# Kernel tuning notes

Measured on AMD Instinct MI355X. Metric: run time of the kernel, lower is better.

Reference implementation:

```python
import jax, jax.numpy as jnp
import numpy as np

KERNEL_MUL = 2.0
KERNEL_NUM = 5


def setup_inputs() -> dict:
    key = jax.random.key(0)
    k1, k2 = jax.random.split(key)
    source = jax.random.normal(k1, (4096, 256), dtype=jnp.float32)
    target = jax.random.normal(k2, (4096, 256), dtype=jnp.float32)
    return {"source": source, "target": target}


def reference(source, target):
    n = source.shape[0]
    m = target.shape[0]
    total = jnp.concatenate([source, target], axis=0)  # [n+m, d]
    N = n + m
    # pairwise squared L2 distances via GEMM identity (same math as expand-based)
    sq = jnp.sum(total * total, axis=1)  # [N]
    d2 = sq[:, None] + sq[None, :] - 2.0 * (total @ total.T)  # [N, N]
    d2 = jnp.maximum(d2, 0.0)
    # bandwidth from detached distances (torch uses L2_distance.data)
    bandwidth = jax.lax.stop_gradient(jnp.sum(d2)) / (N * N - N)
    bandwidth = bandwidth / (KERNEL_MUL ** (KERNEL_NUM // 2))
    kernels = jnp.zeros_like(d2)
    for i in range(KERNEL_NUM):  # fixed small loop over bandwidths
        kernels = kernels + jnp.exp(-d2 / (bandwidth * (KERNEL_MUL ** i)))
    XX = jnp.mean(kernels[:n, :n])
    YY = jnp.mean(kernels[n:, n:])
    XY = jnp.mean(kernels[:n, n:])
    YX = jnp.mean(kernels[n:, :n])
    return XX + YY - XY - YX
```

## Files before the change

kernel.cpp:

```cpp
#include <hip/hip_runtime.h>
#include <hip/hip_bf16.h>
#include <stdint.h>
#include <math.h>

#define D     256
#define NTOT  8192
#define NSRC  4096
#define NT    64
#define NTRI  (NT * (NT + 1) / 2)
#define PREPB 256

using bf16x8 = __attribute__((ext_vector_type(8))) short;
using f32x4  = __attribute__((ext_vector_type(4))) float;

#define GLB_AS __attribute__((address_space(1)))
#define LDS_AS __attribute__((address_space(3)))

#if __has_builtin(__builtin_amdgcn_exp2f)
#define EXP2F __builtin_amdgcn_exp2f
#else
#define EXP2F exp2f
#endif

#define OFF_XB   ((size_t)0)
#define OFF_SQ   ((size_t)NTOT * D * 2)
#define OFF_CP   (OFF_SQ + (size_t)NTOT * 4)
#define OFF_SP   (OFF_CP + (size_t)PREPB * 256 * 4)
#define OFF_CF   (OFF_SP + (size_t)PREPB * 4)
#define OFF_PT   (OFF_CF + 32)
#define OFF_END  (OFF_PT + (size_t)NTRI * 4)

__global__ __launch_bounds__(256) void prep_kernel(
    const float* __restrict__ src, const float* __restrict__ tgt,
    __hip_bfloat16* __restrict__ xb, float* __restrict__ sq,
    float* __restrict__ colpart, float* __restrict__ sqpart)
{
  __shared__ float scol4[4][256];
  __shared__ float sSl[4];
  const int tid = threadIdx.x, wave = tid >> 6, lane = tid & 63;
  const int row0 = blockIdx.x * 32 + wave * 8;
  const float* p0 = (row0 < NSRC) ? (src + (size_t)row0 * D)
                                  : (tgt + (size_t)(row0 - NSRC) * D);
  float c0 = 0.f, c1 = 0.f, c2 = 0.f, c3 = 0.f, swave = 0.f;
  for (int rr = 0; rr < 8; ++rr) {
    const int row = row0 + rr;
    const float4 v = reinterpret_cast<const float4*>(p0 + (size_t)rr * D)[lane];
    const __hip_bfloat16 b0 = __float2bfloat16(v.x), b1 = __float2bfloat16(v.y),
                         b2 = __float2bfloat16(v.z), b3 = __float2bfloat16(v.w);
    ushort4 h;
    h.x = *(const unsigned short*)&b0; h.y = *(const unsigned short*)&b1;
    h.z = *(const unsigned short*)&b2; h.w = *(const unsigned short*)&b3;
    reinterpret_cast<ushort4*>(xb + (size_t)row * D)[lane] = h;
    const float f0 = __bfloat162float(b0), f1 = __bfloat162float(b1),
                f2 = __bfloat162float(b2), f3 = __bfloat162float(b3);
    c0 += f0; c1 += f1; c2 += f2; c3 += f3;
    float s = f0 * f0 + f1 * f1 + f2 * f2 + f3 * f3;
    #pragma unroll
    for (int off = 32; off > 0; off >>= 1) s += __shfl_down(s, off);
    if (lane == 0) { sq[row] = s; swave += s; }
  }
  scol4[wave][lane * 4 + 0] = c0;
  scol4[wave][lane * 4 + 1] = c1;
  scol4[wave][lane * 4 + 2] = c2;
  scol4[wave][lane * 4 + 3] = c3;
  if (lane == 0) sSl[wave] = swave;
  __syncthreads();
  colpart[blockIdx.x * 256 + tid] =
      scol4[0][tid] + scol4[1][tid] + scol4[2][tid] + scol4[3][tid];
  if (tid == 0) sqpart[blockIdx.x] = sSl[0] + sSl[1] + sSl[2] + sSl[3];
}

__global__ __launch_bounds__(256) void bw_kernel(
    const float* __restrict__ colpart, const float* __restrict__ sqpart,
    float* __restrict__ cf)
{
  __shared__ float red[256];
  const int t = threadIdx.x;
  float cs = 0.f;
  for (int b = 0; b < PREPB; ++b) cs += colpart[b * 256 + t];
  red[t] = cs * cs;
  __syncthreads();
  for (int off = 128; off > 0; off >>= 1) {
    if (t < off) red[t] += red[t + off];
    __syncthreads();
  }
  const float s2 = red[0];
  __syncthreads();
  red[t] = (t < PREPB) ? sqpart[t] : 0.f;
  __syncthreads();
  for (int off = 128; off > 0; off >>= 1) {
    if (t < off) red[t] += red[t + off];
    __syncthreads();
  }
  if (t == 0) {
    const double sumd2 = 2.0 * (double)NTOT * (double)red[0] - 2.0 * (double)s2;
    const double bw = sumd2 / ((double)NTOT * (double)NTOT - (double)NTOT) / 4.0;
    cf[0] = (float)(-1.4426950408889634 / (bw * 16.0));
  }
}

__global__ __launch_bounds__(256) void pair_kernel(
    const __hip_bfloat16* __restrict__ xb, const float* __restrict__ sq,
    const float* __restrict__ cf, float* __restrict__ part)
{
  const int idx = (blockIdx.x & 7) * (NTRI / 8) + (blockIdx.x >> 3);
  const float rr = sqrtf(4160.25f - 2.0f * (float)idx);
  int bi = (int)(64.5f - rr);
  while (NT * (bi + 1) - (bi + 1) * bi / 2 <= idx) ++bi;
  while (NT * bi - bi * (bi - 1) / 2 > idx) --bi;
  const int bj = bi + (idx - (NT * bi - bi * (bi - 1) / 2));

  __shared__ __align__(16) short lA[128 * 64];
  __shared__ __align__(16) short lB[128 * 64];
  __shared__ float sqA[128], sqB[128], wsum[4];

  const int tid = threadIdx.x, wave = tid >> 6, lane = tid & 63;
  const int wr = wave >> 1, wc = wave & 1;

  const float c4 = cf[0];
  if (tid < 128) sqA[tid] = sq[bi * 128 + tid];
  else           sqB[tid - 128] = sq[bj * 128 + (tid - 128)];

  const int srow = lane >> 3;
  const int scol_e = ((lane & 7) ^ srow) * 8;
  const __hip_bfloat16* gA = xb + (size_t)(bi * 128 + wave * 8 + srow) * D + scol_e;
  const __hip_bfloat16* gB = xb + (size_t)(bj * 128 + wave * 8 + srow) * D + scol_e;
  char* ldsA = (char*)lA + (wave * 8) * 128;
  char* ldsB = (char*)lB + (wave * 8) * 128;

  f32x4 acc[4][4];
  #pragma unroll
  for (int mi = 0; mi < 4; ++mi)
    #pragma unroll
    for (int nj = 0; nj < 4; ++nj)
      acc[mi][nj] = (f32x4){0.f, 0.f, 0.f, 0.f};

  #pragma unroll
  for (int t = 0; t < 4; ++t) {
    #pragma unroll
    for (int q = 0; q < 4; ++q) {
      __builtin_amdgcn_global_load_lds(
          (const GLB_AS uint32_t*)(gA + (size_t)q * 32 * D + t * 64),
          (LDS_AS uint32_t*)(ldsA + q * 32 * 128), 16, 0, 0);
      __builtin_amdgcn_global_load_lds(
          (const GLB_AS uint32_t*)(gB + (size_t)q * 32 * D + t * 64),
          (LDS_AS uint32_t*)(ldsB + q * 32 * 128), 16, 0, 0);
    }
    __syncthreads();

    #pragma unroll
    for (int ks = 0; ks < 2; ++ks) {
      bf16x8 af[4], bfr[4];
      const int kb = (ks * 32 + (lane >> 4) * 8) * 2;
      #pragma unroll
      for (int mi = 0; mi < 4; ++mi) {
        const int row = wr * 64 + mi * 16 + (lane & 15);
        af[mi] = *(const bf16x8*)((const char*)lA + row * 128 + (kb ^ ((row & 7) << 4)));
      }
      #pragma unroll
      for (int nj = 0; nj < 4; ++nj) {
        const int row = wc * 64 + nj * 16 + (lane & 15);
        bfr[nj] = *(const bf16x8*)((const char*)lB + row * 128 + (kb ^ ((row & 7) << 4)));
      }
      #pragma unroll
      for (int mi = 0; mi < 4; ++mi)
        #pragma unroll
        for (int nj = 0; nj < 4; ++nj)
          acc[mi][nj] = __builtin_amdgcn_mfma_f32_16x16x32_bf16(
              af[mi], bfr[nj], acc[mi][nj], 0, 0, 0);
    }
    if (t < 3) __syncthreads();
  }

  const int r0 = (lane >> 4) * 4, cc = lane & 15;
  float sjv[4];
  #pragma unroll
  for (int nj = 0; nj < 4; ++nj) sjv[nj] = sqB[wc * 64 + nj * 16 + cc];
  float tsum = 0.f;
  #pragma unroll
  for (int mi = 0; mi < 4; ++mi) {
    #pragma unroll
    for (int r = 0; r < 4; ++r) {
      const float si = sqA[wr * 64 + mi * 16 + r0 + r];
      #pragma unroll
      for (int nj = 0; nj < 4; ++nj) {
        float d2 = fmaf(-2.f, acc[mi][nj][r], si + sjv[nj]);
        d2 = fmaxf(d2, 0.f);
        const float e4 = EXP2F(d2 * c4);
        const float e3 = e4 * e4, e2 = e3 * e3;
        const float e1 = e2 * e2, e0 = e1 * e1;
        tsum += ((e4 + e3) + (e2 + e1)) + e0;
      }
    }
  }
  #pragma unroll
  for (int off = 32; off > 0; off >>= 1) tsum += __shfl_down(tsum, off);
  if (lane == 0) wsum[wave] = tsum;
  __syncthreads();
  if (tid == 0) part[idx] = wsum[0] + wsum[1] + wsum[2] + wsum[3];
}

__global__ __launch_bounds__(256) void out_kernel(
    const float* __restrict__ part, float* __restrict__ out)
{
  __shared__ double red0[256], red1[256], red2[256];
  const int t = threadIdx.x;
  double a0 = 0.0, a1 = 0.0, a2 = 0.0;
  for (int j = t; j < NTRI; j += 256) {
    const float r1 = sqrtf(4160.25f - 2.0f * (float)j);
    int bi = (int)(64.5f - r1);
    while (NT * (bi + 1) - (bi + 1) * bi / 2 <= j) ++bi;
    while (NT * bi - bi * (bi - 1) / 2 > j) --bi;
    const int bj = bi + (j - (NT * bi - bi * (bi - 1) / 2));
    const double w = (bi == bj) ? 1.0 : 2.0;
    const double v = w * (double)part[j];
    if (bi >= 32) a1 += v;
    else if (bj >= 32) a2 += v;
    else a0 += v;
  }
  red0[t] = a0; red1[t] = a1; red2[t] = a2;
  __syncthreads();
  for (int off = 128; off > 0; off >>= 1) {
    if (t < off) {
      red0[t] += red0[t + off];
      red1[t] += red1[t + off];
      red2[t] += red2[t + off];
    }
    __syncthreads();
  }
  if (t == 0)
    out[0] = (float)((red0[0] + red1[0] - red2[0]) /
                     ((double)NSRC * (double)NSRC));
}

extern "C" void kernel_launch(void* const* d_in, const int* in_sizes, int n_in,
                              void* d_out, int out_size, void* d_ws, size_t ws_size,
                              hipStream_t stream) {
  (void)in_sizes; (void)n_in; (void)out_size; (void)ws_size;
  const float* src = (const float*)d_in[0];
  const float* tgt = (const float*)d_in[1];
  char* ws = (char*)d_ws;
  __hip_bfloat16* xb = (__hip_bfloat16*)(ws + OFF_XB);
  float* sq      = (float*)(ws + OFF_SQ);
  float* colpart = (float*)(ws + OFF_CP);
  float* sqpart  = (float*)(ws + OFF_SP);
  float* cf      = (float*)(ws + OFF_CF);
  float* part    = (float*)(ws + OFF_PT);

  prep_kernel<<<PREPB, 256, 0, stream>>>(src, tgt, xb, sq, colpart, sqpart);
  bw_kernel<<<1, 256, 0, stream>>>(colpart, sqpart, cf);
  pair_kernel<<<NTRI, 256, 0, stream>>>(xb, sq, cf, part);
  out_kernel<<<1, 256, 0, stream>>>(part, (float*)d_out);
}
```

Baseline: 56.33 us.

## Quantize inputs to FP8 e4m3 and use fp8 MFMA for pairwise Gram tiles

Replaces the bf16 conversion with a software FP8 e4m3 quantizer in the prep kernel, and uses 16x16x32 fp8 MFMA in the pair kernel. Halving the element size halves global and LDS traffic and cuts the K-loop to two stages, with the staging layout and LDS swizzle rewritten for 128-byte rows. Squared norms and column sums are computed from the dequantized values to stay consistent. This costs a lot of precision, because e4m3 has a 3-bit mantissa, so the kernel exponentials and the final MMD value may drift past tolerance.

```diff
diff --git a/kernel.cpp b/kernel.cpp
--- a/kernel.cpp
+++ b/kernel.cpp
@@ -10,8 +10,7 @@
 #define NTRI  (NT * (NT + 1) / 2)
 #define PREPB 256
 
-using bf16x8 = __attribute__((ext_vector_type(8))) short;
-using f32x4  = __attribute__((ext_vector_type(4))) float;
+using f32x4 = __attribute__((ext_vector_type(4))) float;
 
 #define GLB_AS __attribute__((address_space(1)))
 #define LDS_AS __attribute__((address_space(3)))
@@ -22,8 +21,27 @@
 #define EXP2F exp2f
 #endif
 
+__device__ inline unsigned char f32_to_e4m3(float v) {
+  uint32_t u = __float_as_uint(v);
+  uint32_t s = (u >> 24) & 0x80u;
+  uint32_t m = u & 0x7FFFFFFFu;
+  if (m <= 0x3C000000u) return (unsigned char)s;
+  if (m <  0x3C800000u) return (unsigned char)(s | 0x08u);
+  if (m >= 0x43F00000u) return (unsigned char)(s | 0x7Eu);
+  uint32_t r = m + 0x0007FFFFu + ((m >> 20) & 1u);
+  uint32_t e = (r >> 23) - 127u + 7u;
+  return (unsigned char)(s | (e << 3) | ((r >> 20) & 7u));
+}
+__device__ inline float e4m3_to_f32(unsigned char q) {
+  uint32_t s = ((uint32_t)(q & 0x80u)) << 24;
+  uint32_t em = q & 0x7Fu;
+  if (em == 0) return __uint_as_float(s);
+  uint32_t e = (em >> 3) + 120u;
+  return __uint_as_float(s | (e << 23) | ((em & 7u) << 20));
+}
+
 #define OFF_XB   ((size_t)0)
-#define OFF_SQ   ((size_t)NTOT * D * 2)
+#define OFF_SQ   ((size_t)NTOT * D)
 #define OFF_CP   (OFF_SQ + (size_t)NTOT * 4)
 #define OFF_SP   (OFF_CP + (size_t)PREPB * 256 * 4)
 #define OFF_CF   (OFF_SP + (size_t)PREPB * 4)
@@ -32,7 +50,7 @@
 
 __global__ __launch_bounds__(256) void prep_kernel(
     const float* __restrict__ src, const float* __restrict__ tgt,
-    __hip_bfloat16* __restrict__ xb, float* __restrict__ sq,
+    unsigned char* __restrict__ xb, float* __restrict__ sq,
     float* __restrict__ colpart, float* __restrict__ sqpart)
 {
   __shared__ float scol4[4][256];
@@ -45,14 +63,12 @@
   for (int rr = 0; rr < 8; ++rr) {
     const int row = row0 + rr;
     const float4 v = reinterpret_cast<const float4*>(p0 + (size_t)rr * D)[lane];
-    const __hip_bfloat16 b0 = __float2bfloat16(v.x), b1 = __float2bfloat16(v.y),
-                         b2 = __float2bfloat16(v.z), b3 = __float2bfloat16(v.w);
-    ushort4 h;
-    h.x = *(const unsigned short*)&b0; h.y = *(const unsigned short*)&b1;
-    h.z = *(const unsigned short*)&b2; h.w = *(const unsigned short*)&b3;
-    reinterpret_cast<ushort4*>(xb + (size_t)row * D)[lane] = h;
-    const float f0 = __bfloat162float(b0), f1 = __bfloat162float(b1),
-                f2 = __bfloat162float(b2), f3 = __bfloat162float(b3);
+    uchar4 h;
+    h.x = f32_to_e4m3(v.x); h.y = f32_to_e4m3(v.y);
+    h.z = f32_to_e4m3(v.z); h.w = f32_to_e4m3(v.w);
+    reinterpret_cast<uchar4*>(xb + (size_t)row * D)[lane] = h;
+    const float f0 = e4m3_to_f32(h.x), f1 = e4m3_to_f32(h.y),
+                f2 = e4m3_to_f32(h.z), f3 = e4m3_to_f32(h.w);
     c0 += f0; c1 += f1; c2 += f2; c3 += f3;
     float s = f0 * f0 + f1 * f1 + f2 * f2 + f3 * f3;
     #pragma unroll
@@ -100,7 +116,7 @@
 }
 
 __global__ __launch_bounds__(256) void pair_kernel(
-    const __hip_bfloat16* __restrict__ xb, const float* __restrict__ sq,
+    const unsigned char* __restrict__ xb, const float* __restrict__ sq,
     const float* __restrict__ cf, float* __restrict__ part)
 {
   const int idx = (blockIdx.x & 7) * (NTRI / 8) + (blockIdx.x >> 3);
@@ -110,8 +126,8 @@
   while (NT * bi - bi * (bi - 1) / 2 > idx) --bi;
   const int bj = bi + (idx - (NT * bi - bi * (bi - 1) / 2));
 
-  __shared__ __align__(16) short lA[128 * 64];
-  __shared__ __align__(16) short lB[128 * 64];
+  __shared__ __align__(16) unsigned char lA[128 * 128];
+  __shared__ __align__(16) unsigned char lB[128 * 128];
   __shared__ float sqA[128], sqB[128], wsum[4];
 
   const int tid = threadIdx.x, wave = tid >> 6, lane = tid & 63;
@@ -121,12 +137,23 @@
   if (tid < 128) sqA[tid] = sq[bi * 128 + tid];
   else           sqB[tid - 128] = sq[bj * 128 + (tid - 128)];
 
-  const int srow = lane >> 3;
-  const int scol_e = ((lane & 7) ^ srow) * 8;
-  const __hip_bfloat16* gA = xb + (size_t)(bi * 128 + wave * 8 + srow) * D + scol_e;
-  const __hip_bfloat16* gB = xb + (size_t)(bj * 128 + wave * 8 + srow) * D + scol_e;
-  char* ldsA = (char*)lA + (wave * 8) * 128;
-  char* ldsB = (char*)lB + (wave * 8) * 128;
+  const unsigned char* gA0 =
+      xb + (size_t)(bi * 128 + wave * 32 + (lane >> 3)) * D + ((lane & 7) ^ (lane >> 3)) * 16;
+  const unsigned char* gB0 =
+      xb + (size_t)(bj * 128 + wave * 32 + (lane >> 3)) * D + ((lane & 7) ^ (lane >> 3)) * 16;
+  char* dA = (char*)lA + wave * 4096;
+  char* dB = (char*)lB + wave * 4096;
+
+#define STAGE(t) do {                                                        \
+    _Pragma("unroll")                                                        \
+    for (int q = 0; q < 4; ++q) {                                            \
+      __builtin_amdgcn_global_load_lds(                                      \
+          (const GLB_AS uint32_t*)(gA0 + (size_t)q * 8 * D + (t) * 128),     \
+          (LDS_AS uint32_t*)(dA + q * 1024), 16, 0, 0);                      \
+      __builtin_amdgcn_global_load_lds(                                      \
+          (const GLB_AS uint32_t*)(gB0 + (size_t)q * 8 * D + (t) * 128),     \
+          (LDS_AS uint32_t*)(dB + q * 1024), 16, 0, 0);                      \
+    } } while (0)
 
   f32x4 acc[4][4];
   #pragma unroll
@@ -135,44 +162,41 @@
     for (int nj = 0; nj < 4; ++nj)
       acc[mi][nj] = (f32x4){0.f, 0.f, 0.f, 0.f};
 
-  #pragma unroll
-  for (int t = 0; t < 4; ++t) {
-    #pragma unroll
-    for (int q = 0; q < 4; ++q) {
-      __builtin_amdgcn_global_load_lds(
-          (const GLB_AS uint32_t*)(gA + (size_t)q * 32 * D + t * 64),
-          (LDS_AS uint32_t*)(ldsA + q * 32 * 128), 16, 0, 0);
-      __builtin_amdgcn_global_load_lds(
-          (const GLB_AS uint32_t*)(gB + (size_t)q * 32 * D + t * 64),
-          (LDS_AS uint32_t*)(ldsB + q * 32 * 128), 16, 0, 0);
-    }
-    __syncthreads();
-
-    #pragma unroll
-    for (int ks = 0; ks < 2; ++ks) {
-      bf16x8 af[4], bfr[4];
-      const int kb = (ks * 32 + (lane >> 4) * 8) * 2;
+  const int g = lane >> 4, r7 = lane & 7, rlow = lane & 15;
+  const int off8 = (g & 1) * 8, ghalf = g >> 1;
+
+  #pragma unroll
+  for (int t = 0; t < 2; ++t) {
+    STAGE(t);
+    __syncthreads();
+    #pragma unroll
+    for (int ks = 0; ks < 4; ++ks) {
+      const int slot = (2 * ks + ghalf);
+      long af[4], bf[4];
       #pragma unroll
       for (int mi = 0; mi < 4; ++mi) {
-        const int row = wr * 64 + mi * 16 + (lane & 15);
-        af[mi] = *(const bf16x8*)((const char*)lA + row * 128 + (kb ^ ((row & 7) << 4)));
+        const int rowA = wr * 64 + mi * 16 + rlow;
+        af[mi] = *(const long*)((const char*)lA + rowA * 128 +
+                                (((slot ^ r7)) << 4) + off8);
       }
       #pragma unroll
       for (int nj = 0; nj < 4; ++nj) {
-        const int row = wc * 64 + nj * 16 + (lane & 15);
-        bfr[nj] = *(const bf16x8*)((const char*)lB + row * 128 + (kb ^ ((row & 7) << 4)));
+        const int rowB = wc * 64 + nj * 16 + rlow;
+        bf[nj] = *(const long*)((const char*)lB + rowB * 128 +
+                                (((slot ^ r7)) << 4) + off8);
       }
       #pragma unroll
       for (int mi = 0; mi < 4; ++mi)
         #pragma unroll
         for (int nj = 0; nj < 4; ++nj)
-          acc[mi][nj] = __builtin_amdgcn_mfma_f32_16x16x32_bf16(
-              af[mi], bfr[nj], acc[mi][nj], 0, 0, 0);
+          acc[mi][nj] = __builtin_amdgcn_mfma_f32_16x16x32_fp8_fp8(
+              af[mi], bf[nj], acc[mi][nj], 0, 0, 0);
     }
-    if (t < 3) __syncthreads();
-  }
-
-  const int r0 = (lane >> 4) * 4, cc = lane & 15;
+    if (t == 0) __syncthreads();
+  }
+#undef STAGE
+
+  const int r0c = (lane >> 4) * 4, cc = lane & 15;
   float sjv[4];
   #pragma unroll
   for (int nj = 0; nj < 4; ++nj) sjv[nj] = sqB[wc * 64 + nj * 16 + cc];
@@ -181,7 +205,7 @@
   for (int mi = 0; mi < 4; ++mi) {
     #pragma unroll
     for (int r = 0; r < 4; ++r) {
-      const float si = sqA[wr * 64 + mi * 16 + r0 + r];
+      const float si = sqA[wr * 64 + mi * 16 + r0c + r];
       #pragma unroll
       for (int nj = 0; nj < 4; ++nj) {
         float d2 = fmaf(-2.f, acc[mi][nj][r], si + sjv[nj]);
@@ -240,7 +264,7 @@
   const float* src = (const float*)d_in[0];
   const float* tgt = (const float*)d_in[1];
   char* ws = (char*)d_ws;
-  __hip_bfloat16* xb = (__hip_bfloat16*)(ws + OFF_XB);
+  unsigned char* xb = (unsigned char*)(ws + OFF_XB);
   float* sq      = (float*)(ws + OFF_SQ);
   float* colpart = (float*)(ws + OFF_CP);
   float* sqpart  = (float*)(ws + OFF_SP);
```

New measurement: 52.35 us. 1.08x faster.
